# Performance work log

Measured on AMD Instinct MI355X. Metric: run time of the kernel, lower is better.

Reference implementation:

```python
import jax, jax.numpy as jnp
import numpy as np

NUM_EXPERTS = 8
VOCAB_SIZE = 100000
H = 1024
IE = 512  # intermediate_size // num_experts
B, S = 4, 8192


def setup_inputs() -> dict:
    key = jax.random.key(0)
    ks = jax.random.split(key, 8)
    return {
        "hidden_states": jax.random.normal(ks[0], (B, S, H), dtype=jnp.float32),
        "token_ids": jax.random.randint(ks[1], (B, S), 0, VOCAB_SIZE, dtype=jnp.int64),
        "gate_w": jax.random.normal(ks[2], (NUM_EXPERTS, H, IE), dtype=jnp.float32) * 0.02,
        "up_w": jax.random.normal(ks[3], (NUM_EXPERTS, H, IE), dtype=jnp.float32) * 0.02,
        "down_w": jax.random.normal(ks[4], (NUM_EXPERTS, IE, H), dtype=jnp.float32) * 0.02,
        "shared_gate_w": jax.random.normal(ks[5], (IE, H), dtype=jnp.float32) * 0.02,
        "shared_up_w": jax.random.normal(ks[6], (IE, H), dtype=jnp.float32) * 0.02,
        "shared_down_w": jax.random.normal(ks[7], (H, IE), dtype=jnp.float32) * 0.02,
    }


def reference(hidden_states, token_ids, gate_w, up_w, down_w,
              shared_gate_w, shared_up_w, shared_down_w):
    Bq, Sq, Hq = hidden_states.shape
    flat_x = hidden_states.reshape(-1, Hq)                    # [N, H]
    ids = jnp.clip(token_ids, 0, VOCAB_SIZE - 1).reshape(-1)  # [N]
    # token_to_expert buffer is arange(V) % E (no token_frequencies given)
    expert_ids = ids % NUM_EXPERTS                            # [N]

    # shared dense SwiGLU expert (torch Linear: x @ W.T)
    shared_out = (jax.nn.silu(flat_x @ shared_gate_w.T)
                  * (flat_x @ shared_up_w.T)) @ shared_down_w.T

    # routed experts: loop over the small fixed expert set, mask-combine
    routed_out = jnp.zeros_like(flat_x)
    for e in range(NUM_EXPERTS):
        mask = (expert_ids == e)[:, None]                     # [N, 1]
        inter = jax.nn.silu(flat_x @ gate_w[e]) * (flat_x @ up_w[e])  # [N, IE]
        routed_out = routed_out + jnp.where(mask, inter @ down_w[e], 0.0)

    return (routed_out + shared_out).reshape(Bq, Sq, Hq)
```

## Files before the change

kernel.cpp:

```cpp
#include <hip/hip_runtime.h>
#include <hip/hip_bf16.h>


#define N_TOK 32768
#define HD 1024
#define NE 8

typedef __attribute__((ext_vector_type(8))) short bf16x8;
typedef __attribute__((ext_vector_type(8))) unsigned short u16x8;
typedef __attribute__((ext_vector_type(4))) float f32x4;

__device__ __forceinline__ unsigned short f2bf(float f) {
  unsigned int x = __float_as_uint(f);
  x += 0x7fffu + ((x >> 16) & 1u);
  return (unsigned short)(x >> 16);
}

__device__ __forceinline__ void gld16(const unsigned short* g, unsigned short* l) {
  __builtin_amdgcn_global_load_lds(
      (const __attribute__((address_space(1))) unsigned int*)g,
      (__attribute__((address_space(3))) unsigned int*)l,
      16, 0, 0);
}

__device__ __forceinline__ int expert_of(int id) {
  int v = id < 0 ? 0 : (id > 99999 ? 99999 : id);
  return v & 7;
}

__global__ void k_zero(int* ctrl) {
  if (threadIdx.x < 16) ctrl[threadIdx.x] = 0;
}

__global__ void k_count(const int* __restrict__ ids, int* __restrict__ cnt) {
  __shared__ int l[NE];
  if (threadIdx.x < NE) l[threadIdx.x] = 0;
  __syncthreads();
  int t = blockIdx.x * 256 + threadIdx.x;
  atomicAdd(&l[expert_of(ids[t])], 1);
  __syncthreads();
  if (threadIdx.x < NE) atomicAdd(&cnt[threadIdx.x], l[threadIdx.x]);
}

__global__ void k_scan(const int* __restrict__ cnt, int* __restrict__ off) {
  if (threadIdx.x == 0 && blockIdx.x == 0) {
    int a = 0;
    for (int e = 0; e < NE; e++) { off[e] = a; a += (cnt[e] + 127) & ~127; }
    off[NE] = a;
  }
}

__global__ void k_fill(const int* __restrict__ ids, int* __restrict__ cursor,
                       const int* __restrict__ off, int* __restrict__ perm) {
  __shared__ int lcnt[NE], lbase[NE];
  if (threadIdx.x < NE) lcnt[threadIdx.x] = 0;
  __syncthreads();
  int t = blockIdx.x * 256 + threadIdx.x;
  int e = expert_of(ids[t]);
  int r = atomicAdd(&lcnt[e], 1);
  __syncthreads();
  if (threadIdx.x < NE)
    lbase[threadIdx.x] = atomicAdd(&cursor[threadIdx.x], lcnt[threadIdx.x]);
  __syncthreads();
  perm[off[e] + lbase[e] + r] = t;
}

__global__ void k_cvt_x(const float* __restrict__ src, unsigned short* __restrict__ dst) {
  size_t i = ((size_t)blockIdx.x * 256 + threadIdx.x) * 8;
  float4 a = *reinterpret_cast<const float4*>(src + i);
  float4 b = *reinterpret_cast<const float4*>(src + i + 4);
  u16x8 o;
  o[0]=f2bf(a.x); o[1]=f2bf(a.y); o[2]=f2bf(a.z); o[3]=f2bf(a.w);
  o[4]=f2bf(b.x); o[5]=f2bf(b.y); o[6]=f2bf(b.z); o[7]=f2bf(b.w);
  *reinterpret_cast<u16x8*>(dst + i) = o;
}

__device__ __forceinline__ int rowmap(int c, int mode) {
  if (mode == 0) return c;
  return ((c >> 4) << 5) + (c & 15) + (mode == 2 ? 16 : 0);
}

__global__ void k_transpose_cvt(const float* __restrict__ src0, unsigned short* __restrict__ dst0,
                                int C, int mode, size_t src_estride, size_t dst_estride) {
  const float* src = src0 + blockIdx.z * src_estride;
  unsigned short* dst = dst0 + blockIdx.z * dst_estride;
  __shared__ __attribute__((aligned(16))) float tile[32][33];
  int t = threadIdx.x;
  int r0 = blockIdx.y * 32, c0 = blockIdx.x * 32;
  int row = t >> 3, c4 = (t & 7) * 4;
  float4 v = *reinterpret_cast<const float4*>(src + (size_t)(r0 + row) * C + c0 + c4);
  tile[row][c4+0] = v.x; tile[row][c4+1] = v.y; tile[row][c4+2] = v.z; tile[row][c4+3] = v.w;
  __syncthreads();
  ushort4 o;
  o.x = f2bf(tile[c4+0][row]); o.y = f2bf(tile[c4+1][row]);
  o.z = f2bf(tile[c4+2][row]); o.w = f2bf(tile[c4+3][row]);
  int orow = rowmap(c0 + row, mode);
  *reinterpret_cast<ushort4*>(dst + (size_t)orow * HD + r0 + c4) = o;
}

__global__ void k_copy_cvt(const float* __restrict__ src, unsigned short* __restrict__ dst,
                           int cols, int mode, int dcol, size_t dst_estride) {
  size_t i = ((size_t)blockIdx.x * 256 + threadIdx.x) * 4;
  int r = (int)(i / cols), c = (int)(i % cols);
  int row = (mode == 0) ? r : (1024 + rowmap(r, mode));
  float4 v = *reinterpret_cast<const float4*>(src + i);
  ushort4 o; o.x=f2bf(v.x); o.y=f2bf(v.y); o.z=f2bf(v.z); o.w=f2bf(v.w);
  *reinterpret_cast<ushort4*>(dst + blockIdx.z * dst_estride
                              + (size_t)row * HD + dcol + c) = o;
}

__global__ __launch_bounds__(512, 2) void k_gu(
    const unsigned short* __restrict__ xbf,
    const unsigned short* __restrict__ W1,
    const int* __restrict__ perm, const int* __restrict__ cnt, const int* __restrict__ off,
    unsigned short* __restrict__ inter) {
  const int e = blockIdx.z;
  const int ce = cnt[e];
  const int m0 = blockIdx.y * 256;
  if (m0 >= ce) return;
  const int cep = (ce + 127) & ~127;
  const int n0 = blockIdx.x * 256;
  const int oe = off[e];
  __shared__ __attribute__((aligned(16))) unsigned short sm[65536];
  const int tid = threadIdx.x;
  const int lane = tid & 63;
  const int wv = tid >> 6;
  const int wm = wv >> 2, wn = wv & 3;

  const int srow = wv * 16 + (tid & 15);
  const int srck = ((tid >> 4) & 3) * 8;
  int ia = m0 + srow;        if (ia > ce - 1) ia = ce - 1;
  int ib = m0 + 128 + srow;  if (ib > ce - 1) ib = ce - 1;
  const unsigned short* pA0 = xbf + (size_t)perm[oe + ia] * HD + srck;
  const unsigned short* pA1 = xbf + (size_t)perm[oe + ib] * HD + srck;
  const unsigned short* pB0 = W1 + ((size_t)e << 21) + (size_t)(n0 + srow) * HD + srck;
  const unsigned short* pB1 = W1 + ((size_t)e << 21) + (size_t)(n0 + 128 + srow) * HD + srck;

  f32x4 acc[8][4];
#pragma unroll
  for (int mi = 0; mi < 8; mi++)
#pragma unroll
    for (int ni = 0; ni < 4; ni++) acc[mi][ni] = (f32x4){0.f, 0.f, 0.f, 0.f};

  auto stageA = [&](int b, int ks, int kt) {
    unsigned short* d = sm + b * 16384 + ks * 8192 + wv * 512;
    const int ko = kt * 64 + ks * 32;
    gld16(pA0 + ko, d);
    gld16(pA1 + ko, d + 4096);
  };
  auto stageB = [&](int b, int ks, int kt) {
    unsigned short* d = sm + 32768 + b * 16384 + ks * 8192 + wv * 512;
    const int ko = kt * 64 + ks * 32;
    gld16(pB0 + ko, d);
    gld16(pB1 + ko, d + 4096);
  };

  bf16x8 bb[4];
  auto phase = [&](int b, int ks, int mh) {
    asm volatile("s_barrier" ::: "memory");
    const unsigned short* Ar = sm + b * 16384 + ks * 8192;
    if (mh == 0) {
      const unsigned short* Br = sm + 32768 + b * 16384 + ks * 8192;
#pragma unroll
      for (int ni = 0; ni < 4; ni++)
        bb[ni] = *reinterpret_cast<const bf16x8*>(Br + (wn * 4 + ni) * 512 + lane * 8);
    }
    bf16x8 a[4];
#pragma unroll
    for (int j = 0; j < 4; j++)
      a[j] = *reinterpret_cast<const bf16x8*>(Ar + (wm * 8 + mh * 4 + j) * 512 + lane * 8);
    __builtin_amdgcn_s_setprio(1);
#pragma unroll
    for (int j = 0; j < 4; j++)
#pragma unroll
      for (int ni = 0; ni < 4; ni++)
        acc[mh * 4 + j][ni] = __builtin_amdgcn_mfma_f32_16x16x32_bf16(a[j], bb[ni], acc[mh * 4 + j][ni], 0, 0, 0);
    __builtin_amdgcn_s_setprio(0);
    asm volatile("s_barrier" ::: "memory");
  };

  stageA(0, 0, 0); stageB(0, 0, 0); stageA(0, 1, 0); stageB(0, 1, 0);
  stageA(1, 0, 1); stageB(1, 0, 1);
#pragma unroll 1
  for (int j = 0; j < 7; j++) {
    const int t1 = 2 * j + 1, t2 = 2 * j + 2, t3 = 2 * j + 3;
    stageA(1, 1, t1); asm volatile("s_waitcnt vmcnt(10)" ::: "memory"); phase(0, 0, 0);
    stageB(1, 1, t1);                                                   phase(0, 0, 1);
    stageA(0, 0, t2); asm volatile("s_waitcnt vmcnt(10)" ::: "memory"); phase(0, 1, 0);
    stageB(0, 0, t2);                                                   phase(0, 1, 1);
    stageA(0, 1, t2); asm volatile("s_waitcnt vmcnt(10)" ::: "memory"); phase(1, 0, 0);
    stageB(0, 1, t2);                                                   phase(1, 0, 1);
    stageA(1, 0, t3); asm volatile("s_waitcnt vmcnt(10)" ::: "memory"); phase(1, 1, 0);
    stageB(1, 0, t3);                                                   phase(1, 1, 1);
  }
  stageA(1, 1, 15); asm volatile("s_waitcnt vmcnt(10)" ::: "memory"); phase(0, 0, 0);
  stageB(1, 1, 15);                                                   phase(0, 0, 1);
  asm volatile("s_waitcnt vmcnt(8)" ::: "memory");                    phase(0, 1, 0);
                                                                      phase(0, 1, 1);
  asm volatile("s_waitcnt vmcnt(4)" ::: "memory");                    phase(1, 0, 0);
                                                                      phase(1, 0, 1);
  asm volatile("s_waitcnt vmcnt(0)" ::: "memory");                    phase(1, 1, 0);
                                                                      phase(1, 1, 1);

  const int colbase = (n0 + wn * 64) >> 1;
#pragma unroll
  for (int mi = 0; mi < 8; mi++)
#pragma unroll
    for (int p = 0; p < 2; p++)
#pragma unroll
      for (int r = 0; r < 4; r++) {
        int m = wm * 128 + mi * 16 + (lane >> 4) * 4 + r;
        if (m0 + m < cep) {
          float g = acc[mi][2 * p][r];
          float u = acc[mi][2 * p + 1][r];
          float sv = g / (1.f + __expf(-g)) * u;
          inter[(size_t)(oe + m0 + m) * HD + colbase + p * 16 + (lane & 15)] = f2bf(sv);
        }
      }
}

__global__ __launch_bounds__(512, 2) void k_down(
    const unsigned short* __restrict__ inter,
    const unsigned short* __restrict__ Dt,
    const int* __restrict__ perm, const int* __restrict__ cnt, const int* __restrict__ off,
    float* __restrict__ out) {
  const int e = blockIdx.z;
  const int ce = cnt[e];
  const int m0 = blockIdx.y * 256;
  if (m0 >= ce) return;
  const int cep = (ce + 127) & ~127;
  const int n0 = blockIdx.x * 256;
  const int oe = off[e];
  __shared__ __attribute__((aligned(16))) unsigned short sm[65536];
  const int tid = threadIdx.x;
  const int lane = tid & 63;
  const int wv = tid >> 6;
  const int wm = wv >> 2, wn = wv & 3;

  const int srow = wv * 16 + (tid & 15);
  const int srck = ((tid >> 4) & 3) * 8;
  int ia = m0 + srow;        if (ia > cep - 1) ia = cep - 1;
  int ib = m0 + 128 + srow;  if (ib > cep - 1) ib = cep - 1;
  const unsigned short* pA0 = inter + (size_t)(oe + ia) * HD + srck;
  const unsigned short* pA1 = inter + (size_t)(oe + ib) * HD + srck;
  const unsigned short* pB0 = Dt + ((size_t)e << 20) + (size_t)(n0 + srow) * HD + srck;
  const unsigned short* pB1 = Dt + ((size_t)e << 20) + (size_t)(n0 + 128 + srow) * HD + srck;

  f32x4 acc[8][4];
#pragma unroll
  for (int mi = 0; mi < 8; mi++)
#pragma unroll
    for (int ni = 0; ni < 4; ni++) acc[mi][ni] = (f32x4){0.f, 0.f, 0.f, 0.f};

  auto stageA = [&](int b, int ks, int kt) {
    unsigned short* d = sm + b * 16384 + ks * 8192 + wv * 512;
    const int ko = kt * 64 + ks * 32;
    gld16(pA0 + ko, d);
    gld16(pA1 + ko, d + 4096);
  };
  auto stageB = [&](int b, int ks, int kt) {
    unsigned short* d = sm + 32768 + b * 16384 + ks * 8192 + wv * 512;
    const int ko = kt * 64 + ks * 32;
    gld16(pB0 + ko, d);
    gld16(pB1 + ko, d + 4096);
  };

  bf16x8 bb[4];
  auto phase = [&](int b, int ks, int mh) {
    asm volatile("s_barrier" ::: "memory");
    const unsigned short* Ar = sm + b * 16384 + ks * 8192;
    if (mh == 0) {
      const unsigned short* Br = sm + 32768 + b * 16384 + ks * 8192;
#pragma unroll
      for (int ni = 0; ni < 4; ni++)
        bb[ni] = *reinterpret_cast<const bf16x8*>(Br + (wn * 4 + ni) * 512 + lane * 8);
    }
    bf16x8 a[4];
#pragma unroll
    for (int j = 0; j < 4; j++)
      a[j] = *reinterpret_cast<const bf16x8*>(Ar + (wm * 8 + mh * 4 + j) * 512 + lane * 8);
    __builtin_amdgcn_s_setprio(1);
#pragma unroll
    for (int j = 0; j < 4; j++)
#pragma unroll
      for (int ni = 0; ni < 4; ni++)
        acc[mh * 4 + j][ni] = __builtin_amdgcn_mfma_f32_16x16x32_bf16(a[j], bb[ni], acc[mh * 4 + j][ni], 0, 0, 0);
    __builtin_amdgcn_s_setprio(0);
    asm volatile("s_barrier" ::: "memory");
  };

  stageA(0, 0, 0); stageB(0, 0, 0); stageA(0, 1, 0); stageB(0, 1, 0);
  stageA(1, 0, 1); stageB(1, 0, 1);
#pragma unroll 1
  for (int j = 0; j < 7; j++) {
    const int t1 = 2 * j + 1, t2 = 2 * j + 2, t3 = 2 * j + 3;
    stageA(1, 1, t1); asm volatile("s_waitcnt vmcnt(10)" ::: "memory"); phase(0, 0, 0);
    stageB(1, 1, t1);                                                   phase(0, 0, 1);
    stageA(0, 0, t2); asm volatile("s_waitcnt vmcnt(10)" ::: "memory"); phase(0, 1, 0);
    stageB(0, 0, t2);                                                   phase(0, 1, 1);
    stageA(0, 1, t2); asm volatile("s_waitcnt vmcnt(10)" ::: "memory"); phase(1, 0, 0);
    stageB(0, 1, t2);                                                   phase(1, 0, 1);
    stageA(1, 0, t3); asm volatile("s_waitcnt vmcnt(10)" ::: "memory"); phase(1, 1, 0);
    stageB(1, 0, t3);                                                   phase(1, 1, 1);
  }
  stageA(1, 1, 15); asm volatile("s_waitcnt vmcnt(10)" ::: "memory"); phase(0, 0, 0);
  stageB(1, 1, 15);                                                   phase(0, 0, 1);
  asm volatile("s_waitcnt vmcnt(8)" ::: "memory");                    phase(0, 1, 0);
                                                                      phase(0, 1, 1);
  asm volatile("s_waitcnt vmcnt(4)" ::: "memory");                    phase(1, 0, 0);
                                                                      phase(1, 0, 1);
  asm volatile("s_waitcnt vmcnt(0)" ::: "memory");                    phase(1, 1, 0);
                                                                      phase(1, 1, 1);

#pragma unroll
  for (int mi = 0; mi < 8; mi++)
#pragma unroll
    for (int r = 0; r < 4; r++) {
      int m = wm * 128 + mi * 16 + (lane >> 4) * 4 + r;
      int gm = m0 + m;
      if (gm < ce) {
        int t = perm[oe + gm];
#pragma unroll
        for (int ni = 0; ni < 4; ni++)
          out[(size_t)t * HD + n0 + wn * 64 + ni * 16 + (lane & 15)] = acc[mi][ni][r];
      }
    }
}

__global__ __launch_bounds__(256) void k_naive(
    const float* __restrict__ x, const int* __restrict__ ids,
    const float* __restrict__ gw, const float* __restrict__ uw, const float* __restrict__ dw,
    const float* __restrict__ sgw, const float* __restrict__ suw, const float* __restrict__ sdw,
    float* __restrict__ out) {
  const int t = blockIdx.x;
  const int tid = threadIdx.x;
  __shared__ float sx[1024];
  __shared__ float si[1024];
  for (int i = tid; i < 1024; i += 256) sx[i] = x[(size_t)t * 1024 + i];
  const int e = expert_of(ids[t]);
  __syncthreads();
  const float* gwe = gw + (size_t)e * 1024 * 512;
  const float* uwe = uw + (size_t)e * 1024 * 512;
  for (int j = tid; j < 512; j += 256) {
    float g = 0, u = 0, sg = 0, su = 0;
    for (int k = 0; k < 1024; k++) {
      float xv = sx[k];
      g += xv * gwe[(size_t)k * 512 + j];
      u += xv * uwe[(size_t)k * 512 + j];
      sg += xv * sgw[(size_t)j * 1024 + k];
      su += xv * suw[(size_t)j * 1024 + k];
    }
    si[j] = g / (1.f + __expf(-g)) * u;
    si[512 + j] = sg / (1.f + __expf(-sg)) * su;
  }
  __syncthreads();
  const float* dwe = dw + (size_t)e * 512 * 1024;
  for (int n = tid; n < 1024; n += 256) {
    float a = 0;
    for (int k = 0; k < 512; k++)
      a += si[k] * dwe[(size_t)k * 1024 + n] + si[512 + k] * sdw[(size_t)n * 512 + k];
    out[(size_t)t * 1024 + n] = a;
  }
}

extern "C" void kernel_launch(void* const* d_in, const int* in_sizes, int n_in,
                              void* d_out, int out_size, void* d_ws, size_t ws_size,
                              hipStream_t stream) {
  const float* x = (const float*)d_in[0];
  const int* ids = (const int*)d_in[1];
  const float* gw = (const float*)d_in[2];
  const float* uw = (const float*)d_in[3];
  const float* dw = (const float*)d_in[4];
  const float* sgw = (const float*)d_in[5];
  const float* suw = (const float*)d_in[6];
  const float* sdw = (const float*)d_in[7];
  float* out = (float*)d_out;

  const size_t REQ = 186908672ull;
  if (ws_size < REQ) {
    k_naive<<<N_TOK, 256, 0, stream>>>(x, ids, gw, uw, dw, sgw, suw, sdw, out);
    return;
  }

  char* ws = (char*)d_ws;
  int* ctrl = (int*)ws;
  int* perm = (int*)(ws + 1024);
  unsigned short* xbf = (unsigned short*)(ws + 262144);
  unsigned short* W1 = (unsigned short*)(ws + 67371008ull);
  unsigned short* Dt = (unsigned short*)(ws + 100925440ull);
  unsigned short* inter = (unsigned short*)(ws + 117702656ull);

  k_zero<<<1, 64, 0, stream>>>(ctrl);
  k_count<<<128, 256, 0, stream>>>(ids, ctrl);
  k_scan<<<1, 64, 0, stream>>>(ctrl, ctrl + 16);
  k_fill<<<128, 256, 0, stream>>>(ids, ctrl + 8, ctrl + 16, perm);
  k_cvt_x<<<16384, 256, 0, stream>>>(x, xbf);
  k_transpose_cvt<<<dim3(16, 32, 8), 256, 0, stream>>>(gw, W1, 512, 1,
                                                       (size_t)1024 * 512, (size_t)1 << 21);
  k_transpose_cvt<<<dim3(16, 32, 8), 256, 0, stream>>>(uw, W1, 512, 2,
                                                       (size_t)1024 * 512, (size_t)1 << 21);
  k_transpose_cvt<<<dim3(32, 16, 8), 256, 0, stream>>>(dw, Dt, 1024, 0,
                                                       (size_t)512 * 1024, (size_t)1 << 20);
  k_copy_cvt<<<dim3(512, 1, 8), 256, 0, stream>>>(sgw, W1, 1024, 1, 0, (size_t)1 << 21);
  k_copy_cvt<<<dim3(512, 1, 8), 256, 0, stream>>>(suw, W1, 1024, 2, 0, (size_t)1 << 21);
  k_copy_cvt<<<dim3(512, 1, 8), 256, 0, stream>>>(sdw, Dt, 512, 0, 512, (size_t)1 << 20);
  k_gu<<<dim3(8, 128, 8), 512, 0, stream>>>(xbf, W1, perm, ctrl, ctrl + 16, inter);
  k_down<<<dim3(4, 128, 8), 512, 0, stream>>>(inter, Dt, perm, ctrl, ctrl + 16, out);
}
```

Before: 396.2 us.

## Double-buffer LDS fragment reads in registers to overlap with MFMA

Both GEMM kernels now hold the A and B fragments in two register sets (X/Y). The LDS reads for the next phase are issued right after the current phase's MFMAs, so they run under the matrix work instead of in front of it. The vmcnt waits are moved to match. This costs extra VGPRs for the second fragment set, which may lower occupancy or cause spills, and it makes the barrier and wait placement more delicate to keep correct.

```diff
diff --git a/kernel.cpp b/kernel.cpp
--- a/kernel.cpp
+++ b/kernel.cpp
@@ -9,6 +9,9 @@
 typedef __attribute__((ext_vector_type(8))) short bf16x8;
 typedef __attribute__((ext_vector_type(8))) unsigned short u16x8;
 typedef __attribute__((ext_vector_type(4))) float f32x4;
+
+#define BAR() asm volatile("s_barrier" ::: "memory")
+#define VM8() asm volatile("s_waitcnt vmcnt(8)" ::: "memory")
 
 __device__ __forceinline__ unsigned short f2bf(float f) {
   unsigned int x = __float_as_uint(f);
@@ -154,21 +157,19 @@
     gld16(pB0 + ko, d);
     gld16(pB1 + ko, d + 4096);
   };
-
-  bf16x8 bb[4];
-  auto phase = [&](int b, int ks, int mh) {
-    asm volatile("s_barrier" ::: "memory");
+  auto rdA = [&](bf16x8* dst, int b, int ks, int mh) {
     const unsigned short* Ar = sm + b * 16384 + ks * 8192;
-    if (mh == 0) {
-      const unsigned short* Br = sm + 32768 + b * 16384 + ks * 8192;
-#pragma unroll
-      for (int ni = 0; ni < 4; ni++)
-        bb[ni] = *reinterpret_cast<const bf16x8*>(Br + (wn * 4 + ni) * 512 + lane * 8);
-    }
-    bf16x8 a[4];
 #pragma unroll
     for (int j = 0; j < 4; j++)
-      a[j] = *reinterpret_cast<const bf16x8*>(Ar + (wm * 8 + mh * 4 + j) * 512 + lane * 8);
+      dst[j] = *reinterpret_cast<const bf16x8*>(Ar + (wm * 8 + mh * 4 + j) * 512 + lane * 8);
+  };
+  auto rdB = [&](bf16x8* dst, int b, int ks) {
+    const unsigned short* Br = sm + 32768 + b * 16384 + ks * 8192;
+#pragma unroll
+    for (int ni = 0; ni < 4; ni++)
+      dst[ni] = *reinterpret_cast<const bf16x8*>(Br + (wn * 4 + ni) * 512 + lane * 8);
+  };
+  auto mf = [&](int mh, const bf16x8* a, const bf16x8* bb) {
     __builtin_amdgcn_s_setprio(1);
 #pragma unroll
     for (int j = 0; j < 4; j++)
@@ -176,31 +177,37 @@
       for (int ni = 0; ni < 4; ni++)
         acc[mh * 4 + j][ni] = __builtin_amdgcn_mfma_f32_16x16x32_bf16(a[j], bb[ni], acc[mh * 4 + j][ni], 0, 0, 0);
     __builtin_amdgcn_s_setprio(0);
-    asm volatile("s_barrier" ::: "memory");
-  };
+  };
+
+  bf16x8 aX[4], aY[4], bbX[4], bbY[4];
 
   stageA(0, 0, 0); stageB(0, 0, 0); stageA(0, 1, 0); stageB(0, 1, 0);
   stageA(1, 0, 1); stageB(1, 0, 1);
+  VM8(); BAR();
+  rdA(aX, 0, 0, 0); rdB(bbX, 0, 0);
+
 #pragma unroll 1
   for (int j = 0; j < 7; j++) {
     const int t1 = 2 * j + 1, t2 = 2 * j + 2, t3 = 2 * j + 3;
-    stageA(1, 1, t1); asm volatile("s_waitcnt vmcnt(10)" ::: "memory"); phase(0, 0, 0);
-    stageB(1, 1, t1);                                                   phase(0, 0, 1);
-    stageA(0, 0, t2); asm volatile("s_waitcnt vmcnt(10)" ::: "memory"); phase(0, 1, 0);
-    stageB(0, 0, t2);                                                   phase(0, 1, 1);
-    stageA(0, 1, t2); asm volatile("s_waitcnt vmcnt(10)" ::: "memory"); phase(1, 0, 0);
-    stageB(0, 1, t2);                                                   phase(1, 0, 1);
-    stageA(1, 0, t3); asm volatile("s_waitcnt vmcnt(10)" ::: "memory"); phase(1, 1, 0);
-    stageB(1, 0, t3);                                                   phase(1, 1, 1);
-  }
-  stageA(1, 1, 15); asm volatile("s_waitcnt vmcnt(10)" ::: "memory"); phase(0, 0, 0);
-  stageB(1, 1, 15);                                                   phase(0, 0, 1);
-  asm volatile("s_waitcnt vmcnt(8)" ::: "memory");                    phase(0, 1, 0);
-                                                                      phase(0, 1, 1);
-  asm volatile("s_waitcnt vmcnt(4)" ::: "memory");                    phase(1, 0, 0);
-                                                                      phase(1, 0, 1);
-  asm volatile("s_waitcnt vmcnt(0)" ::: "memory");                    phase(1, 1, 0);
-                                                                      phase(1, 1, 1);
+    stageA(1,1,t1);        BAR(); mf(0, aX, bbX); rdA(aY,0,0,1);                  BAR();
+    stageB(1,1,t1); VM8(); BAR(); mf(1, aY, bbX); rdA(aX,0,1,0); rdB(bbY,0,1);    BAR();
+    stageA(0,0,t2);        BAR(); mf(0, aX, bbY); rdA(aY,0,1,1);                  BAR();
+    stageB(0,0,t2); VM8(); BAR(); mf(1, aY, bbY); rdA(aX,1,0,0); rdB(bbX,1,0);    BAR();
+    stageA(0,1,t2);        BAR(); mf(0, aX, bbX); rdA(aY,1,0,1);                  BAR();
+    stageB(0,1,t2); VM8(); BAR(); mf(1, aY, bbX); rdA(aX,1,1,0); rdB(bbY,1,1);    BAR();
+    stageA(1,0,t3);        BAR(); mf(0, aX, bbY); rdA(aY,1,1,1);                  BAR();
+    stageB(1,0,t3); VM8(); BAR(); mf(1, aY, bbY); rdA(aX,0,0,0); rdB(bbX,0,0);    BAR();
+  }
+  stageA(1,1,15);        BAR(); mf(0, aX, bbX); rdA(aY,0,0,1);                  BAR();
+  stageB(1,1,15); VM8(); BAR(); mf(1, aY, bbX); rdA(aX,0,1,0); rdB(bbY,0,1);    BAR();
+                         BAR(); mf(0, aX, bbY); rdA(aY,0,1,1);                  BAR();
+  asm volatile("s_waitcnt vmcnt(4)" ::: "memory");
+                         BAR(); mf(1, aY, bbY); rdA(aX,1,0,0); rdB(bbX,1,0);    BAR();
+                         BAR(); mf(0, aX, bbX); rdA(aY,1,0,1);                  BAR();
+  asm volatile("s_waitcnt vmcnt(0)" ::: "memory");
+                         BAR(); mf(1, aY, bbX); rdA(aX,1,1,0); rdB(bbY,1,1);    BAR();
+                         BAR(); mf(0, aX, bbY); rdA(aY,1,1,1);                  BAR();
+                         BAR(); mf(1, aY, bbY);
 
   const int colbase = (n0 + wn * 64) >> 1;
 #pragma unroll
@@ -264,21 +271,19 @@
     gld16(pB0 + ko, d);
     gld16(pB1 + ko, d + 4096);
   };
-
-  bf16x8 bb[4];
-  auto phase = [&](int b, int ks, int mh) {
-    asm volatile("s_barrier" ::: "memory");
+  auto rdA = [&](bf16x8* dst, int b, int ks, int mh) {
     const unsigned short* Ar = sm + b * 16384 + ks * 8192;
-    if (mh == 0) {
-      const unsigned short* Br = sm + 32768 + b * 16384 + ks * 8192;
-#pragma unroll
-      for (int ni = 0; ni < 4; ni++)
-        bb[ni] = *reinterpret_cast<const bf16x8*>(Br + (wn * 4 + ni) * 512 + lane * 8);
-    }
-    bf16x8 a[4];
 #pragma unroll
     for (int j = 0; j < 4; j++)
-      a[j] = *reinterpret_cast<const bf16x8*>(Ar + (wm * 8 + mh * 4 + j) * 512 + lane * 8);
+      dst[j] = *reinterpret_cast<const bf16x8*>(Ar + (wm * 8 + mh * 4 + j) * 512 + lane * 8);
+  };
+  auto rdB = [&](bf16x8* dst, int b, int ks) {
+    const unsigned short* Br = sm + 32768 + b * 16384 + ks * 8192;
+#pragma unroll
+    for (int ni = 0; ni < 4; ni++)
+      dst[ni] = *reinterpret_cast<const bf16x8*>(Br + (wn * 4 + ni) * 512 + lane * 8);
+  };
+  auto mf = [&](int mh, const bf16x8* a, const bf16x8* bb) {
     __builtin_amdgcn_s_setprio(1);
 #pragma unroll
     for (int j = 0; j < 4; j++)
@@ -286,31 +291,37 @@
       for (int ni = 0; ni < 4; ni++)
         acc[mh * 4 + j][ni] = __builtin_amdgcn_mfma_f32_16x16x32_bf16(a[j], bb[ni], acc[mh * 4 + j][ni], 0, 0, 0);
     __builtin_amdgcn_s_setprio(0);
-    asm volatile("s_barrier" ::: "memory");
-  };
+  };
+
+  bf16x8 aX[4], aY[4], bbX[4], bbY[4];
 
   stageA(0, 0, 0); stageB(0, 0, 0); stageA(0, 1, 0); stageB(0, 1, 0);
   stageA(1, 0, 1); stageB(1, 0, 1);
+  VM8(); BAR();
+  rdA(aX, 0, 0, 0); rdB(bbX, 0, 0);
+
 #pragma unroll 1
   for (int j = 0; j < 7; j++) {
     const int t1 = 2 * j + 1, t2 = 2 * j + 2, t3 = 2 * j + 3;
-    stageA(1, 1, t1); asm volatile("s_waitcnt vmcnt(10)" ::: "memory"); phase(0, 0, 0);
-    stageB(1, 1, t1);                                                   phase(0, 0, 1);
-    stageA(0, 0, t2); asm volatile("s_waitcnt vmcnt(10)" ::: "memory"); phase(0, 1, 0);
-    stageB(0, 0, t2);                                                   phase(0, 1, 1);
-    stageA(0, 1, t2); asm volatile("s_waitcnt vmcnt(10)" ::: "memory"); phase(1, 0, 0);
-    stageB(0, 1, t2);                                                   phase(1, 0, 1);
-    stageA(1, 0, t3); asm volatile("s_waitcnt vmcnt(10)" ::: "memory"); phase(1, 1, 0);
-    stageB(1, 0, t3);                                                   phase(1, 1, 1);
-  }
-  stageA(1, 1, 15); asm volatile("s_waitcnt vmcnt(10)" ::: "memory"); phase(0, 0, 0);
-  stageB(1, 1, 15);                                                   phase(0, 0, 1);
-  asm volatile("s_waitcnt vmcnt(8)" ::: "memory");                    phase(0, 1, 0);
-                                                                      phase(0, 1, 1);
-  asm volatile("s_waitcnt vmcnt(4)" ::: "memory");                    phase(1, 0, 0);
-                                                                      phase(1, 0, 1);
-  asm volatile("s_waitcnt vmcnt(0)" ::: "memory");                    phase(1, 1, 0);
-                                                                      phase(1, 1, 1);
+    stageA(1,1,t1);        BAR(); mf(0, aX, bbX); rdA(aY,0,0,1);                  BAR();
+    stageB(1,1,t1); VM8(); BAR(); mf(1, aY, bbX); rdA(aX,0,1,0); rdB(bbY,0,1);    BAR();
+    stageA(0,0,t2);        BAR(); mf(0, aX, bbY); rdA(aY,0,1,1);                  BAR();
+    stageB(0,0,t2); VM8(); BAR(); mf(1, aY, bbY); rdA(aX,1,0,0); rdB(bbX,1,0);    BAR();
+    stageA(0,1,t2);        BAR(); mf(0, aX, bbX); rdA(aY,1,0,1);                  BAR();
+    stageB(0,1,t2); VM8(); BAR(); mf(1, aY, bbX); rdA(aX,1,1,0); rdB(bbY,1,1);    BAR();
+    stageA(1,0,t3);        BAR(); mf(0, aX, bbY); rdA(aY,1,1,1);                  BAR();
+    stageB(1,0,t3); VM8(); BAR(); mf(1, aY, bbY); rdA(aX,0,0,0); rdB(bbX,0,0);    BAR();
+  }
+  stageA(1,1,15);        BAR(); mf(0, aX, bbX); rdA(aY,0,0,1);                  BAR();
+  stageB(1,1,15); VM8(); BAR(); mf(1, aY, bbX); rdA(aX,0,1,0); rdB(bbY,0,1);    BAR();
+                         BAR(); mf(0, aX, bbY); rdA(aY,0,1,1);                  BAR();
+  asm volatile("s_waitcnt vmcnt(4)" ::: "memory");
+                         BAR(); mf(1, aY, bbY); rdA(aX,1,0,0); rdB(bbX,1,0);    BAR();
+                         BAR(); mf(0, aX, bbX); rdA(aY,1,0,1);                  BAR();
+  asm volatile("s_waitcnt vmcnt(0)" ::: "memory");
+                         BAR(); mf(1, aY, bbX); rdA(aX,1,1,0); rdB(bbY,1,1);    BAR();
+                         BAR(); mf(0, aX, bbY); rdA(aY,1,1,1);                  BAR();
+                         BAR(); mf(1, aY, bbY);
 
 #pragma unroll
   for (int mi = 0; mi < 8; mi++)
```

Measured after the change: 391.0 us. No clear change (-1.3%).
